# Kernel optimization log

Hardware: AMD Instinct MI355X
Metric: run time of the kernel (lower is better)

## Reference

```python
import jax, jax.numpy as jnp
import numpy as np

B, T, D = 2, 1024, 2048
H, KV, Dh = 16, 4, 128
REP = H // KV
LAMBDA_INIT = 0.8 - 0.6 * float(np.exp(-0.3 * 0))  # depth=0 -> 0.2
ROPE_THETA = 10000.0


def rope_cos_sin(pos, dh):
    # standard rotary embedding tables, half-split (rotate_half) convention
    inv_freq = 1.0 / (ROPE_THETA ** (jnp.arange(0, dh, 2, dtype=jnp.float32) / dh))
    freqs = pos.astype(jnp.float32)[:, None] * inv_freq[None, :]  # (T, Dh/2)
    return jnp.cos(freqs), jnp.sin(freqs)


def apply_rope(x, cos, sin):
    # x: (B, H, T, Dh); cos/sin: (T, Dh/2)
    x1, x2 = jnp.split(x, 2, axis=-1)
    c = cos[None, None, :, :]
    s = sin[None, None, :, :]
    return jnp.concatenate([x1 * c - x2 * s, x1 * s + x2 * c], axis=-1)


def setup_inputs() -> dict:
    key = jax.random.key(0)
    ks = jax.random.split(key, 5)
    std = 0.02
    return {
        "x": jax.random.normal(ks[0], (B, T, D), dtype=jnp.float32),
        "wq": jax.random.normal(ks[1], (D, 2 * H * Dh), dtype=jnp.float32) * std,
        "wk": jax.random.normal(ks[2], (D, 2 * KV * Dh), dtype=jnp.float32) * std,
        "wv": jax.random.normal(ks[3], (D, 2 * KV * Dh), dtype=jnp.float32) * std,
        "wo": jax.random.normal(ks[4], (2 * H * Dh, D), dtype=jnp.float32) * std,
    }


def reference(x, wq, wk, wv, wo):
    # projections (no bias)
    q = (x @ wq).reshape(B, T, H, 2 * Dh).transpose(0, 2, 1, 3)    # (B,H,T,2Dh)
    k = (x @ wk).reshape(B, T, KV, 2 * Dh).transpose(0, 2, 1, 3)   # (B,KV,T,2Dh)
    v = (x @ wv).reshape(B, T, KV, 2 * Dh).transpose(0, 2, 1, 3)   # (B,KV,T,2Dh)

    q1, q2 = jnp.split(q, 2, axis=-1)
    k1, k2 = jnp.split(k, 2, axis=-1)

    pos = jnp.arange(T)
    cos, sin = rope_cos_sin(pos, Dh)
    q1 = apply_rope(q1, cos, sin)
    q2 = apply_rope(q2, cos, sin)
    k1 = apply_rope(k1, cos, sin)
    k2 = apply_rope(k2, cos, sin)

    # GQA: repeat kv heads contiguously (matches expand+reshape)
    k1f = jnp.repeat(k1, REP, axis=1)
    k2f = jnp.repeat(k2, REP, axis=1)
    vf = jnp.repeat(v, REP, axis=1)  # (B,H,T,2Dh)

    scale = 1.0 / jnp.sqrt(jnp.float32(Dh))
    scores1 = jnp.einsum("bhtd,bhsd->bhts", q1, k1f) * scale
    scores2 = jnp.einsum("bhtd,bhsd->bhts", q2, k2f) * scale

    causal = jnp.triu(jnp.ones((T, T), dtype=bool), k=1)  # True above diagonal
    neg_inf = jnp.float32(-jnp.inf)
    scores1 = jnp.where(causal[None, None], neg_inf, scores1)
    scores2 = jnp.where(causal[None, None], neg_inf, scores2)

    attn1 = jax.nn.softmax(scores1, axis=-1)
    attn2 = jax.nn.softmax(scores2, axis=-1)
    attn_diff = attn1 - LAMBDA_INIT * attn2

    out = jnp.einsum("bhts,bhsd->bhtd", attn_diff, vf)  # (B,H,T,2Dh)
    out = out.transpose(0, 2, 1, 3).reshape(B, T, 2 * H * Dh)
    return out @ wo  # (B,T,D)
```

## Files before the change

kernel.cpp:

```cpp
#include <hip/hip_runtime.h>
#include <hip/hip_bf16.h>
#include <stdint.h>

typedef __bf16 bf16_t;
typedef __attribute__((ext_vector_type(8))) __bf16 bf16x8;
typedef __attribute__((ext_vector_type(4))) __bf16 bf16x4;
typedef __attribute__((ext_vector_type(4))) float f32x4;

#define AS1 __attribute__((address_space(1)))
#define AS3 __attribute__((address_space(3)))

__device__ inline void gload_lds16(const void* g, void* l) {
    __builtin_amdgcn_global_load_lds((AS1 void*)(uintptr_t)g, (AS3 void*)l, 16, 0, 0);
}

__device__ inline f32x4 mfma_bf16_16x16x32(bf16x8 a, bf16x8 b, f32x4 c) {
    return __builtin_amdgcn_mfma_f32_16x16x32_bf16(a, b, c, 0, 0, 0);
}


__global__ __launch_bounds__(256) void cast_x_kernel(const float* __restrict__ x,
                                                     bf16_t* __restrict__ xb, int n) {
    int i = (blockIdx.x * 256 + threadIdx.x) * 4;
    if (i >= n) return;
    float4 v = *reinterpret_cast<const float4*>(x + i);
    bf16x4 o;
    o[0] = (bf16_t)v.x; o[1] = (bf16_t)v.y; o[2] = (bf16_t)v.z; o[3] = (bf16_t)v.w;
    *reinterpret_cast<bf16x4*>(xb + i) = o;
}

__global__ __launch_bounds__(256) void transpose_cast_w(const float* __restrict__ s0,
                                                        const float* __restrict__ s1,
                                                        const float* __restrict__ s2,
                                                        int n1, int n2,
                                                        int ld0, int ld1, int ld2,
                                                        int K, int N, bf16_t* __restrict__ dst) {
    __shared__ float tile[32][33];
    const int kt = blockIdx.x * 32, nt = blockIdx.y * 32;
    const int tx = threadIdx.x & 31, ty = threadIdx.x >> 5;
    #pragma unroll
    for (int j = 0; j < 4; j++) {
        int k = kt + ty + j * 8;
        int n = nt + tx;
        float v;
        if (n < n1)      v = s0[(size_t)k * ld0 + n];
        else if (n < n2) v = s1[(size_t)k * ld1 + (n - n1)];
        else             v = s2[(size_t)k * ld2 + (n - n2)];
        tile[ty + j * 8][tx] = v;
    }
    __syncthreads();
    #pragma unroll
    for (int j = 0; j < 4; j++) {
        int n = nt + ty + j * 8;
        int k = kt + tx;
        dst[(size_t)n * K + k] = (bf16_t)tile[tx][ty + j * 8];
    }
}

__global__ __launch_bounds__(256) void pack_vt(const bf16_t* __restrict__ qkv,
                                               bf16_t* __restrict__ vt) {
    __shared__ bf16_t tile[32][33];
    const int st = blockIdx.x * 32, dt = blockIdx.y * 32, bkv = blockIdx.z;
    const int b = bkv >> 2, kv = bkv & 3;
    const int tx = threadIdx.x & 31, ty = threadIdx.x >> 5;
    #pragma unroll
    for (int j = 0; j < 4; j++) {
        int s = st + ty + j * 8;
        tile[ty + j * 8][tx] = qkv[(size_t)(b * 1024 + s) * 6144 + 5120 + kv * 256 + dt + tx];
    }
    __syncthreads();
    #pragma unroll
    for (int j = 0; j < 4; j++) {
        int d = dt + ty + j * 8;
        vt[(size_t)(bkv * 256 + d) * 1024 + st + tx] = tile[tx][ty + j * 8];
    }
}

__global__ __launch_bounds__(256) void combine_splitk(const float* __restrict__ p,
                                                      float* __restrict__ out, int n) {
    int i = (blockIdx.x * 256 + threadIdx.x) * 4;
    if (i >= n) return;
    float4 a = *reinterpret_cast<const float4*>(p + i);
    float4 b = *reinterpret_cast<const float4*>(p + n + i);
    float4 o;
    o.x = a.x + b.x; o.y = a.y + b.y; o.z = a.z + b.z; o.w = a.w + b.w;
    *reinterpret_cast<float4*>(out + i) = o;
}

template <int BN, int OUT_BF16, int ROPE, int SPLITK>
__global__ __launch_bounds__(256, 3) void gemm_bt(const bf16_t* __restrict__ A,
                                                  const bf16_t* __restrict__ Bt,
                                                  void* __restrict__ Cv,
                                                  int M, int N, int K) {
    constexpr int ASZ = 128 * 32;
    constexpr int BSZ = BN * 32;
    constexpr int MI = (BN == 128) ? 4 : 2;
    __shared__ bf16_t As[2 * ASZ];
    __shared__ bf16_t Bs[2 * BSZ];
    const int tid = threadIdx.x;
    const int w = tid >> 6, l = tid & 63;
    const int lq = l & 15, g = l >> 4;
    const int wrow = (BN == 128) ? ((w >> 1) * 64) : (w * 32);
    const int wn = (BN == 128) ? (w & 1) : 0;
    const int lin = blockIdx.x;
    const int chunk = gridDim.x >> 3;
    const int swz = (lin & 7) * chunk + (lin >> 3);
    int tile = swz, split = 0;
    if constexpr (SPLITK > 1) {
        const int tiles = gridDim.x / SPLITK;
        split = swz / tiles;
        tile = swz % tiles;
    }
    const size_t m0 = (size_t)(tile & 15) * 128;
    const size_t n0 = (size_t)(tile >> 4) * BN;
    const int KS = K / SPLITK;
    f32x4 acc[MI][4];
    #pragma unroll
    for (int i = 0; i < MI; i++)
        #pragma unroll
        for (int j = 0; j < 4; j++) { acc[i][j][0] = 0.f; acc[i][j][1] = 0.f; acc[i][j][2] = 0.f; acc[i][j][3] = 0.f; }
    const int rowi = l >> 2;
    const int ko = (l & 3) * 8;
    const bf16_t* Ab = A + (m0 + rowi) * K + ko + (size_t)split * KS;
    const bf16_t* Bb = Bt + (n0 + rowi) * K + ko + (size_t)split * KS;
    const int nt = KS / 32;

    auto colInTile = [&](int ni) {
        return (BN == 128) ? (wn * 16 + ni * 32 + lq) : (ni * 16 + lq);
    };

    auto stage = [&](int buf, int t) {
        const int k0 = t * 32;
        #pragma unroll
        for (int j = 0; j < 2; j++) {
            const int c = j * 4 + w;
            gload_lds16(Ab + (size_t)(c * 16) * K + k0, As + buf * ASZ + c * 512);
        }
        if constexpr (BN == 128) {
            #pragma unroll
            for (int j = 0; j < 2; j++) {
                const int c = j * 4 + w;
                gload_lds16(Bb + (size_t)(c * 16) * K + k0, Bs + buf * BSZ + c * 512);
            }
        } else {
            gload_lds16(Bb + (size_t)(w * 16) * K + k0, Bs + buf * BSZ + w * 512);
        }
    };

    stage(0, 0);
    __syncthreads();
    int cur = 0;
    for (int t = 0; t < nt; t++) {
        if (t + 1 < nt) stage(cur ^ 1, t + 1);
        bf16x8 af[MI], bfv[4];
        #pragma unroll
        for (int mi = 0; mi < MI; mi++)
            af[mi] = *reinterpret_cast<const bf16x8*>(&As[cur * ASZ + (wrow + mi * 16 + lq) * 32 + g * 8]);
        #pragma unroll
        for (int ni = 0; ni < 4; ni++)
            bfv[ni] = *reinterpret_cast<const bf16x8*>(&Bs[cur * BSZ + colInTile(ni) * 32 + g * 8]);
        #pragma unroll
        for (int mi = 0; mi < MI; mi++)
            #pragma unroll
            for (int ni = 0; ni < 4; ni++)
                acc[mi][ni] = mfma_bf16_16x16x32(af[mi], bfv[ni], acc[mi][ni]);
        __syncthreads();
        cur ^= 1;
    }

    if constexpr (ROPE) {
        if (n0 < 5120) {
            #pragma unroll
            for (int ni = 0; ni < 2; ni++) {
                const int i = wn * 16 + ni * 32 + lq;
                const float invf = exp2f(-0.20762050593045893f * (float)i);
                #pragma unroll
                for (int mi = 0; mi < MI; mi++)
                    #pragma unroll
                    for (int r = 0; r < 4; r++) {
                        const int row = (int)m0 + wrow + mi * 16 + 4 * g + r;
                        const float a = (float)(row & 1023) * invf;
                        const float c = __cosf(a), s = __sinf(a);
                        const float x1 = acc[mi][ni][r], x2 = acc[mi][ni + 2][r];
                        acc[mi][ni][r]     = x1 * c - x2 * s;
                        acc[mi][ni + 2][r] = x1 * s + x2 * c;
                    }
            }
        }
    }

    float* outf = (float*)Cv + (size_t)split * M * N;
    #pragma unroll
    for (int mi = 0; mi < MI; mi++)
        #pragma unroll
        for (int ni = 0; ni < 4; ni++)
            #pragma unroll
            for (int r = 0; r < 4; r++) {
                size_t row = m0 + wrow + mi * 16 + 4 * g + r;
                size_t col = n0 + colInTile(ni);
                float v = acc[mi][ni][r];
                if (OUT_BF16) ((bf16_t*)Cv)[row * N + col] = (bf16_t)v;
                else          outf[row * N + col] = v;
            }
}

__global__ __launch_bounds__(256, 3) void attn_fused(const bf16_t* __restrict__ qkv,
                                                     const bf16_t* __restrict__ vt,
                                                     bf16_t* __restrict__ ao) {
    const int bid = blockIdx.x;
    const int u = bid >> 3;
    const int bh = (bid & 7) * 4 + (u & 3);
    const int qtr = u >> 2;
    const int qt = qtr ^ ((qtr & 8) ? 7 : 0);
    const int b = bh >> 4, h = bh & 15, kv = h >> 2;
    const int tid = threadIdx.x;
    const int w = tid >> 6, l = tid & 63;
    const int rg = w >> 1, wh = w & 1;
    const int lq = l & 15, g = l >> 4;
    const int q0 = qt * 32;
    const float scale = 0.08838834764831845f;
    const float FIXM = 6.0f;

    __shared__ char smem[16384 + 16384 + 4 * 1280];
    bf16_t* Ks  = (bf16_t*)smem;
    bf16_t* Vs  = (bf16_t*)(smem + 16384);
    bf16_t* Ps  = (bf16_t*)(smem + 32768) + w * 640;
    bf16_t* O2s = (bf16_t*)smem;

    bf16x8 qf[4];
    {
        const bf16_t* qp = qkv + (size_t)(b * 1024 + q0 + rg * 16 + lq) * 6144 + h * 256 + wh * 128 + g * 8;
        #pragma unroll
        for (int c = 0; c < 4; c++) qf[c] = *reinterpret_cast<const bf16x8*>(qp + c * 32);
    }
    const int t = q0 + rg * 16 + lq;

    const int kr_off = l >> 5;
    const int kc16   = l & 31;
    const int vd_off = l >> 2;
    const int vc16   = l & 3;

    const bf16_t* kgbase = qkv + (size_t)(b * 1024) * 6144 + 4096 + kv * 256;
    const bf16_t* vgbase = vt + (size_t)((b * 4 + kv) * 256) * 1024;

    float lsum = 0.f;
    f32x4 oacc[16];
    #pragma unroll
    for (int dt = 0; dt < 16; dt++) { oacc[dt][0] = 0.f; oacc[dt][1] = 0.f; oacc[dt][2] = 0.f; oacc[dt][3] = 0.f; }

    const int nr = qt + 1;
    for (int rnd = 0; rnd < nr; ++rnd) {
        const int s0 = rnd * 32;
        #pragma unroll
        for (int j = 0; j < 4; j++) {
            int r = 8 * w + 2 * j + kr_off;
            int d = (kc16 ^ (r & 7)) * 8;
            gload_lds16(kgbase + (size_t)(s0 + r) * 6144 + d, Ks + (8 * w + 2 * j) * 256);
        }
        #pragma unroll
        for (int j = 0; j < 4; j++) {
            int d = 64 * w + 16 * j + vd_off;
            int sc = (vc16 ^ ((d >> 1) & 3)) * 8;
            gload_lds16(vgbase + (size_t)d * 1024 + s0 + sc, Vs + (64 * w + 16 * j) * 32);
        }
        __syncthreads();

        f32x4 stA, stB;
        stA[0] = stA[1] = stA[2] = stA[3] = 0.f;
        stB[0] = stB[1] = stB[2] = stB[3] = 0.f;
        __builtin_amdgcn_s_setprio(1);
        #pragma unroll
        for (int c = 0; c < 4; c++) {
            const int c16 = wh * 16 + c * 4 + g;
            const int rA = lq, rB = 16 + lq;
            bf16x8 kfa = *reinterpret_cast<const bf16x8*>(Ks + rA * 256 + ((c16 ^ (rA & 7)) * 8));
            bf16x8 kfb = *reinterpret_cast<const bf16x8*>(Ks + rB * 256 + ((c16 ^ (rB & 7)) * 8));
            stA = mfma_bf16_16x16x32(kfa, qf[c], stA);
            stB = mfma_bf16_16x16x32(kfb, qf[c], stB);
        }
        __builtin_amdgcn_s_setprio(0);

        const bool lastr = (rnd == nr - 1);
        float pA[4], pB[4];
        #pragma unroll
        for (int r = 0; r < 4; r++) {
            float a  = fmaf(stA[r], scale, -FIXM);
            float bv = fmaf(stB[r], scale, -FIXM);
            if (lastr) {
                if (s0 + 4 * g + r > t)      a  = -1e30f;
                if (s0 + 16 + 4 * g + r > t) bv = -1e30f;
            }
            pA[r] = __expf(a);
            pB[r] = __expf(bv);
            lsum += pA[r] + pB[r];
        }

        bf16x4 wa, wb;
        #pragma unroll
        for (int r = 0; r < 4; r++) { wa[r] = (bf16_t)pA[r]; wb[r] = (bf16_t)pB[r]; }
        *reinterpret_cast<bf16x4*>(&Ps[lq * 40 + 4 * g]) = wa;
        *reinterpret_cast<bf16x4*>(&Ps[lq * 40 + 16 + 4 * g]) = wb;
        bf16x8 pf = *reinterpret_cast<const bf16x8*>(&Ps[lq * 40 + 8 * g]);
        __builtin_amdgcn_s_setprio(1);
        #pragma unroll
        for (int dt = 0; dt < 16; dt++) {
            const int d = dt * 16 + lq;
            bf16x8 vf = *reinterpret_cast<const bf16x8*>(Vs + d * 32 + ((g ^ ((d >> 1) & 3)) * 8));
            oacc[dt] = mfma_bf16_16x16x32(pf, vf, oacc[dt]);
        }
        __builtin_amdgcn_s_setprio(0);
        __syncthreads();
    }

    lsum += __shfl_xor(lsum, 16);
    lsum += __shfl_xor(lsum, 32);
    float li[4];
    #pragma unroll
    for (int r = 0; r < 4; r++) li[r] = 1.0f / __shfl(lsum, 4 * g + r);

    if (wh == 1) {
        #pragma unroll
        for (int dt = 0; dt < 16; dt++)
            #pragma unroll
            for (int r = 0; r < 4; r++)
                O2s[(rg * 16 + 4 * g + r) * 256 + dt * 16 + lq] = (bf16_t)(oacc[dt][r] * li[r]);
    }
    __syncthreads();
    if (wh == 0) {
        #pragma unroll
        for (int dt = 0; dt < 16; dt++)
            #pragma unroll
            for (int r = 0; r < 4; r++) {
                const int qloc = rg * 16 + 4 * g + r;
                float o2 = (float)O2s[qloc * 256 + dt * 16 + lq];
                ao[(size_t)(b * 1024 + q0 + qloc) * 4096 + h * 256 + dt * 16 + lq] =
                    (bf16_t)(oacc[dt][r] * li[r] - 0.2f * o2);
            }
    }
}


extern "C" void kernel_launch(void* const* d_in, const int* in_sizes, int n_in,
                              void* d_out, int out_size, void* d_ws, size_t ws_size,
                              hipStream_t stream) {
    (void)in_sizes; (void)n_in; (void)out_size;
    const float* x  = (const float*)d_in[0];
    const float* wq = (const float*)d_in[1];
    const float* wk = (const float*)d_in[2];
    const float* wv = (const float*)d_in[3];
    const float* wo = (const float*)d_in[4];

    char* ws = (char*)d_ws;
    size_t off = 0;
    auto alloc = [&](size_t bytes) {
        void* p = ws + off;
        off += (bytes + 255) & ~(size_t)255;
        return p;
    };
    bf16_t* xb   = (bf16_t*)alloc(4194304ull * 2);
    bf16_t* wbt  = (bf16_t*)alloc(6144ull * 2048 * 2);
    bf16_t* wot  = (bf16_t*)alloc(2048ull * 4096 * 2);
    bf16_t* qkvb = (bf16_t*)alloc(2048ull * 6144 * 2);
    bf16_t* vtb  = (bf16_t*)alloc(8ull * 256 * 1024 * 2);
    bf16_t* ao   = (bf16_t*)alloc(2048ull * 4096 * 2);
    if (off > ws_size) return;
    float* psum = (float*)ws;

    cast_x_kernel<<<4096, 256, 0, stream>>>(x, xb, 4194304);
    transpose_cast_w<<<dim3(64, 192), 256, 0, stream>>>(wq, wk, wv, 4096, 5120,
                                                        4096, 1024, 1024, 2048, 6144, wbt);
    transpose_cast_w<<<dim3(128, 64), 256, 0, stream>>>(wo, wo, wo, 1 << 28, 1 << 28,
                                                        2048, 2048, 2048, 4096, 2048, wot);
    gemm_bt<128, 1, 1, 1><<<768, 256, 0, stream>>>(xb, wbt, qkvb, 2048, 6144, 2048);
    pack_vt<<<dim3(32, 8, 8), 256, 0, stream>>>(qkvb, vtb);
    attn_fused<<<1024, 256, 0, stream>>>(qkvb, vtb, ao);
    gemm_bt<64, 0, 0, 2><<<1024, 256, 0, stream>>>(ao, wot, psum, 2048, 2048, 4096);
    combine_splitk<<<4096, 256, 0, stream>>>(psum, (float*)d_out, 4194304);
}
```

Measured before the change: 202.6 us.

## Split long causal attention tiles across two blocks with a combine kernel

Query tiles in the upper half of the causal range (qt 16..31) now have their key rounds split across two workgroups. Each writes unnormalized partial outputs and row sums to workspace, and a new attn_combine kernel merges them. The fixed-max softmax makes the partials directly additive. The goal is to balance the triangular causal workload and reduce the long tail of the biggest tiles, at the cost of an extra launch and partial-result traffic. Tile-to-XCD mapping is also changed so each XCD handles one batch and KV head.

```diff
diff --git a/kernel.cpp b/kernel.cpp
--- a/kernel.cpp
+++ b/kernel.cpp
@@ -85,6 +85,39 @@
     float4 o;
     o.x = a.x + b.x; o.y = a.y + b.y; o.z = a.z + b.z; o.w = a.w + b.w;
     *reinterpret_cast<float4*>(out + i) = o;
+}
+
+__global__ __launch_bounds__(256) void attn_combine(const bf16_t* __restrict__ pO,
+                                                    const float* __restrict__ Ls,
+                                                    bf16_t* __restrict__ ao) {
+    const int tile = blockIdx.x;
+    const int bh = tile >> 4, qtm = tile & 15;
+    const int b = bh >> 4, h = bh & 15;
+    const int q = threadIdx.x >> 3;
+    const int dbase = (threadIdx.x & 7) * 32;
+    const float l0 = Ls[((size_t)(tile * 2 + 0) * 2 + 0) * 32 + q] +
+                     Ls[((size_t)(tile * 2 + 1) * 2 + 0) * 32 + q];
+    const float l1 = Ls[((size_t)(tile * 2 + 0) * 2 + 1) * 32 + q] +
+                     Ls[((size_t)(tile * 2 + 1) * 2 + 1) * 32 + q];
+    const float i0 = 1.0f / l0, i1 = 1.0f / l1;
+    const bf16_t* p00 = pO + ((size_t)(tile * 2 + 0) * 2 + 0) * 8192 + q * 256 + dbase;
+    const bf16_t* p10 = pO + ((size_t)(tile * 2 + 1) * 2 + 0) * 8192 + q * 256 + dbase;
+    const bf16_t* p01 = pO + ((size_t)(tile * 2 + 0) * 2 + 1) * 8192 + q * 256 + dbase;
+    const bf16_t* p11 = pO + ((size_t)(tile * 2 + 1) * 2 + 1) * 8192 + q * 256 + dbase;
+    bf16_t* out = ao + (size_t)(b * 1024 + (16 + qtm) * 32 + q) * 4096 + h * 256 + dbase;
+    #pragma unroll
+    for (int dd = 0; dd < 32; dd += 8) {
+        bf16x8 a0 = *reinterpret_cast<const bf16x8*>(p00 + dd);
+        bf16x8 a1 = *reinterpret_cast<const bf16x8*>(p10 + dd);
+        bf16x8 b0 = *reinterpret_cast<const bf16x8*>(p01 + dd);
+        bf16x8 b1 = *reinterpret_cast<const bf16x8*>(p11 + dd);
+        bf16x8 o;
+        #pragma unroll
+        for (int j = 0; j < 8; j++)
+            o[j] = (bf16_t)(((float)a0[j] + (float)a1[j]) * i0 -
+                            0.2f * (((float)b0[j] + (float)b1[j]) * i1));
+        *reinterpret_cast<bf16x8*>(out + dd) = o;
+    }
 }
 
 template <int BN, int OUT_BF16, int ROPE, int SPLITK>
@@ -206,13 +239,27 @@
 
 __global__ __launch_bounds__(256, 3) void attn_fused(const bf16_t* __restrict__ qkv,
                                                      const bf16_t* __restrict__ vt,
-                                                     bf16_t* __restrict__ ao) {
+                                                     bf16_t* __restrict__ ao,
+                                                     bf16_t* __restrict__ pOut,
+                                                     float* __restrict__ Lsq) {
     const int bid = blockIdx.x;
+    const int xcd = bid & 7;
     const int u = bid >> 3;
-    const int bh = (bid & 7) * 4 + (u & 3);
-    const int qtr = u >> 2;
-    const int qt = qtr ^ ((qtr & 8) ? 7 : 0);
-    const int b = bh >> 4, h = bh & 15, kv = h >> 2;
+    const int hg = u & 3;
+    const int wk = u >> 2;
+    const int b = xcd >> 2, kv = xcd & 3;
+    const int h = kv * 4 + hg;
+    int qt, part, r0, r1, split;
+    if (wk < 32) {
+        const int j = wk >> 1;
+        qt = 31 - j; part = wk & 1; split = 1;
+        const int h1 = (qt + 2) >> 1;
+        r0 = part ? h1 : 0;
+        r1 = part ? (qt + 1) : h1;
+    } else {
+        qt = 47 - wk; part = 0; split = 0;
+        r0 = 0; r1 = qt + 1;
+    }
     const int tid = threadIdx.x;
     const int w = tid >> 6, l = tid & 63;
     const int rg = w >> 1, wh = w & 1;
@@ -248,8 +295,7 @@
     #pragma unroll
     for (int dt = 0; dt < 16; dt++) { oacc[dt][0] = 0.f; oacc[dt][1] = 0.f; oacc[dt][2] = 0.f; oacc[dt][3] = 0.f; }
 
-    const int nr = qt + 1;
-    for (int rnd = 0; rnd < nr; ++rnd) {
+    for (int rnd = r0; rnd < r1; ++rnd) {
         const int s0 = rnd * 32;
         #pragma unroll
         for (int j = 0; j < 4; j++) {
@@ -280,7 +326,7 @@
         }
         __builtin_amdgcn_s_setprio(0);
 
-        const bool lastr = (rnd == nr - 1);
+        const bool lastr = (rnd == qt);
         float pA[4], pB[4];
         #pragma unroll
         for (int r = 0; r < 4; r++) {
@@ -314,28 +360,40 @@
 
     lsum += __shfl_xor(lsum, 16);
     lsum += __shfl_xor(lsum, 32);
-    float li[4];
-    #pragma unroll
-    for (int r = 0; r < 4; r++) li[r] = 1.0f / __shfl(lsum, 4 * g + r);
-
-    if (wh == 1) {
+
+    if (!split) {
+        float li[4];
+        #pragma unroll
+        for (int r = 0; r < 4; r++) li[r] = 1.0f / __shfl(lsum, 4 * g + r);
+        if (wh == 1) {
+            #pragma unroll
+            for (int dt = 0; dt < 16; dt++)
+                #pragma unroll
+                for (int r = 0; r < 4; r++)
+                    O2s[(rg * 16 + 4 * g + r) * 256 + dt * 16 + lq] = (bf16_t)(oacc[dt][r] * li[r]);
+        }
+        __syncthreads();
+        if (wh == 0) {
+            #pragma unroll
+            for (int dt = 0; dt < 16; dt++)
+                #pragma unroll
+                for (int r = 0; r < 4; r++) {
+                    const int qloc = rg * 16 + 4 * g + r;
+                    float o2 = (float)O2s[qloc * 256 + dt * 16 + lq];
+                    ao[(size_t)(b * 1024 + q0 + qloc) * 4096 + h * 256 + dt * 16 + lq] =
+                        (bf16_t)(oacc[dt][r] * li[r] - 0.2f * o2);
+                }
+        }
+    } else {
+        const int tile_lin = (b * 16 + h) * 16 + (qt - 16);
+        bf16_t* po = pOut + ((size_t)(tile_lin * 2 + part) * 2 + wh) * 8192;
         #pragma unroll
         for (int dt = 0; dt < 16; dt++)
             #pragma unroll
             for (int r = 0; r < 4; r++)
-                O2s[(rg * 16 + 4 * g + r) * 256 + dt * 16 + lq] = (bf16_t)(oacc[dt][r] * li[r]);
-    }
-    __syncthreads();
-    if (wh == 0) {
-        #pragma unroll
-        for (int dt = 0; dt < 16; dt++)
-            #pragma unroll
-            for (int r = 0; r < 4; r++) {
-                const int qloc = rg * 16 + 4 * g + r;
-                float o2 = (float)O2s[qloc * 256 + dt * 16 + lq];
-                ao[(size_t)(b * 1024 + q0 + qloc) * 4096 + h * 256 + dt * 16 + lq] =
-                    (bf16_t)(oacc[dt][r] * li[r] - 0.2f * o2);
-            }
+                po[(rg * 16 + 4 * g + r) * 256 + dt * 16 + lq] = (bf16_t)oacc[dt][r];
+        if (l < 16)
+            Lsq[((size_t)(tile_lin * 2 + part) * 2 + wh) * 32 + rg * 16 + lq] = lsum;
     }
 }
 
@@ -363,8 +421,10 @@
     bf16_t* qkvb = (bf16_t*)alloc(2048ull * 6144 * 2);
     bf16_t* vtb  = (bf16_t*)alloc(8ull * 256 * 1024 * 2);
     bf16_t* ao   = (bf16_t*)alloc(2048ull * 4096 * 2);
+    float*  lsq  = (float*)alloc(512ull * 2 * 2 * 32 * 4);
     if (off > ws_size) return;
-    float* psum = (float*)ws;
+    bf16_t* pO   = (bf16_t*)ws;
+    float*  psum = (float*)ws;
 
     cast_x_kernel<<<4096, 256, 0, stream>>>(x, xb, 4194304);
     transpose_cast_w<<<dim3(64, 192), 256, 0, stream>>>(wq, wk, wv, 4096, 5120,
@@ -373,7 +433,8 @@
                                                         2048, 2048, 2048, 4096, 2048, wot);
     gemm_bt<128, 1, 1, 1><<<768, 256, 0, stream>>>(xb, wbt, qkvb, 2048, 6144, 2048);
     pack_vt<<<dim3(32, 8, 8), 256, 0, stream>>>(qkvb, vtb);
-    attn_fused<<<1024, 256, 0, stream>>>(qkvb, vtb, ao);
+    attn_fused<<<1536, 256, 0, stream>>>(qkvb, vtb, ao, pO, lsq);
+    attn_combine<<<512, 256, 0, stream>>>(pO, lsq, ao);
     gemm_bt<64, 0, 0, 2><<<1024, 256, 0, stream>>>(ao, wot, psum, 2048, 2048, 4096);
     combine_splitk<<<4096, 256, 0, stream>>>(psum, (float*)d_out, 4194304);
 }
```

Measured after the change: 214.4 us. 5.9% more time.
